# Kernel tuning notes

Hardware: AMD Instinct MI355X
Metric: run time of the kernel (lower is better)

Reference implementation:

```python
import jax, jax.numpy as jnp
import numpy as np

B, N, DIM_IN, DIM_OUT, CHEB_K, EMBED_DIM = 64, 2048, 64, 64, 3, 10


def setup_inputs() -> dict:
    key = jax.random.key(0)
    k1, k2, k3, k4 = jax.random.split(key, 4)
    x = jax.random.normal(k1, (B, N, DIM_IN), dtype=jnp.float32)
    node_embeddings = jax.random.normal(k2, (N, EMBED_DIM), dtype=jnp.float32)
    # xavier-normal-like init for the pools
    w_std = (2.0 / (EMBED_DIM * CHEB_K * DIM_IN + DIM_OUT)) ** 0.5
    b_std = (2.0 / (EMBED_DIM + DIM_OUT)) ** 0.5
    weights_pool = jax.random.normal(k3, (EMBED_DIM, CHEB_K, DIM_IN, DIM_OUT), dtype=jnp.float32) * w_std
    bias_pool = jax.random.normal(k4, (EMBED_DIM, DIM_OUT), dtype=jnp.float32) * b_std
    return {"x": x, "node_embeddings": node_embeddings,
            "weights_pool": weights_pool, "bias_pool": bias_pool,
            "cheb_k": CHEB_K}


def reference(x, node_embeddings, weights_pool, bias_pool, cheb_k):
    n = node_embeddings.shape[0]
    # adaptive adjacency: softmax(relu(E E^T)) over neighbors
    supports = jax.nn.softmax(jax.nn.relu(node_embeddings @ node_embeddings.T), axis=1)
    # Chebyshev polynomial supports: T0 = I, T1 = A, Tk = 2 A T_{k-1} - T_{k-2}
    support_set = [jnp.eye(n, dtype=supports.dtype), supports]
    for _ in range(2, cheb_k):
        support_set.append(2.0 * supports @ support_set[-1] - support_set[-2])
    supports_k = jnp.stack(support_set, axis=0)  # [K, N, N]
    # per-node weights and bias synthesized from node embeddings
    weights = jnp.einsum('nd,dkio->nkio', node_embeddings, weights_pool)  # [N, K, I, O]
    bias = node_embeddings @ bias_pool                                    # [N, O]
    # graph convolution
    x_g = jnp.einsum('knm,bmc->bnkc', supports_k, x)                      # [B, N, K, I]
    out = jnp.einsum('bnki,nkio->bno', x_g, weights) + bias               # [B, N, O]
    return out
```

## Files before the change

kernel.cpp:

```cpp
#include <hip/hip_runtime.h>

#define NN 2048
#define BB 64
#define CC 64
#define ED 10
#define KK 3
#define JJ (BB * CC)

typedef unsigned short ushort_t;
typedef __attribute__((ext_vector_type(8))) short short8;
typedef __attribute__((ext_vector_type(4))) float f32x4;

typedef const __attribute__((address_space(1))) unsigned* gptr_t;
typedef __attribute__((address_space(3))) unsigned* lptr_t;

static __device__ __forceinline__ ushort_t f2bf(float f) {
    union { float f; unsigned u; } x{f};
    unsigned r = x.u + 0x7FFF + ((x.u >> 16) & 1);
    return (ushort_t)(r >> 16);
}
static __device__ __forceinline__ float bf2f(ushort_t h) {
    union { unsigned u; float f; } x;
    x.u = ((unsigned)h) << 16;
    return x.f;
}

__global__ __launch_bounds__(256) void prep_kernel(const float* __restrict__ E,
                                                   const float* __restrict__ x,
                                                   const float* __restrict__ Wp,
                                                   ushort_t* __restrict__ Ab,
                                                   ushort_t* __restrict__ xT,
                                                   ushort_t* __restrict__ xN,
                                                   ushort_t* __restrict__ WpT) {
    const int bid = blockIdx.x;
    const int tid = threadIdx.x;

    __shared__ float tb[64][68];
    __shared__ float red[8];

    if (bid < NN) {
        const int n = bid;
        float en[ED];
#pragma unroll
        for (int d = 0; d < ED; ++d) en[d] = E[n * ED + d];

        float sv[NN / 256];
        float lmax = 0.0f;
#pragma unroll
        for (int j = 0; j < NN / 256; ++j) {
            const int m = tid + j * 256;
            const float* Em = E + m * ED;
            float dot = 0.0f;
#pragma unroll
            for (int d = 0; d < ED; ++d) dot += en[d] * Em[d];
            float s = fmaxf(dot, 0.0f);
            sv[j] = s;
            lmax = fmaxf(lmax, s);
        }
#pragma unroll
        for (int off = 32; off > 0; off >>= 1) lmax = fmaxf(lmax, __shfl_down(lmax, off, 64));
        if ((tid & 63) == 0) red[tid >> 6] = lmax;
        __syncthreads();
        const float bmax = fmaxf(fmaxf(red[0], red[1]), fmaxf(red[2], red[3]));

        float lsum = 0.0f;
#pragma unroll
        for (int j = 0; j < NN / 256; ++j) {
            sv[j] = __expf(sv[j] - bmax);
            lsum += sv[j];
        }
#pragma unroll
        for (int off = 32; off > 0; off >>= 1) lsum += __shfl_down(lsum, off, 64);
        if ((tid & 63) == 0) red[4 + (tid >> 6)] = lsum;
        __syncthreads();
        const float inv = 1.0f / (red[4] + red[5] + red[6] + red[7]);

#pragma unroll
        for (int j = 0; j < NN / 256; ++j) {
            Ab[(size_t)n * NN + tid + j * 256] = f2bf(sv[j] * inv);
        }
    } else if (bid < 2 * NN) {
        const int t = bid - NN;
        const int n0 = (t & 31) * 64;
        const int b = t >> 5;

#pragma unroll
        for (int l = 0; l < 4; ++l) {
            const int idx = tid + l * 256;
            const int nn = idx >> 4;
            const int c4 = (idx & 15) << 2;
            const float4 v = *(const float4*)(x + ((size_t)b * NN + n0 + nn) * CC + c4);
            tb[c4 + 0][nn] = v.x;
            tb[c4 + 1][nn] = v.y;
            tb[c4 + 2][nn] = v.z;
            tb[c4 + 3][nn] = v.w;
        }
        __syncthreads();

#pragma unroll
        for (int l = 0; l < 2; ++l) {
            const int idx = tid + l * 256;
            const int c = idx >> 3;
            const int ch = (idx & 7) << 3;
            ushort_t pack[8];
#pragma unroll
            for (int e = 0; e < 8; ++e) pack[e] = f2bf(tb[c][ch + e]);
            *(float4*)(xT + (size_t)(b * 64 + c) * NN + n0 + ch) = *(float4*)pack;
        }
#pragma unroll
        for (int l = 0; l < 2; ++l) {
            const int idx = tid + l * 256;
            const int nn = idx >> 3;
            const int cg = (idx & 7) << 3;
            ushort_t pack[8];
#pragma unroll
            for (int e = 0; e < 8; ++e) pack[e] = f2bf(tb[cg + e][nn]);
            *(float4*)(xN + (size_t)(n0 + nn) * JJ + b * 64 + cg) = *(float4*)pack;
        }
    } else {
        const int dk = bid - 2 * NN;
        const float* src = Wp + (size_t)dk * CC * CC;

#pragma unroll
        for (int l = 0; l < 4; ++l) {
            const int idx = tid + l * 256;
            const int i = idx >> 4;
            const int o4 = (idx & 15) << 2;
            const float4 v = *(const float4*)(src + i * CC + o4);
            tb[o4 + 0][i] = v.x;
            tb[o4 + 1][i] = v.y;
            tb[o4 + 2][i] = v.z;
            tb[o4 + 3][i] = v.w;
        }
        __syncthreads();

#pragma unroll
        for (int l = 0; l < 2; ++l) {
            const int idx = tid + l * 256;
            const int o = idx >> 3;
            const int ic = (idx & 7) << 3;
            ushort_t pack[8];
#pragma unroll
            for (int e = 0; e < 8; ++e) pack[e] = f2bf(tb[o][ic + e]);
            *(float4*)(WpT + (size_t)dk * CC * CC + o * CC + ic) = *(float4*)pack;
        }
    }
}

template <int MODE>
__global__ __launch_bounds__(256) void gemm_nt(const ushort_t* __restrict__ A,
                                               const ushort_t* __restrict__ Bt,
                                               const ushort_t* __restrict__ Zn,
                                               ushort_t* __restrict__ Ct,
                                               ushort_t* __restrict__ Cn) {
    const int j0 = blockIdx.x * 128;
    const int m0 = blockIdx.y * 128;
    const int tid = threadIdx.x;
    const int lane = tid & 63;
    const int l16 = lane & 15;
    const int quad = lane >> 4;
    const int w = tid >> 6;
    const int wm = (w >> 1) * 64;
    const int wj = (w & 1) * 64;
    const int lr = lane >> 3;
    const int lc = lane & 7;
    const int swz = lc ^ lr;

    __shared__ ushort_t As[2][128 * 64];
    __shared__ ushort_t Bs[2][128 * 64];

    f32x4 acc[4][4];
#pragma unroll
    for (int mi = 0; mi < 4; ++mi)
#pragma unroll
        for (int ji = 0; ji < 4; ++ji) acc[mi][ji] = (f32x4){0.f, 0.f, 0.f, 0.f};

#pragma unroll
    for (int inst = 0; inst < 4; ++inst) {
        const int rbase = w * 32 + inst * 8;
        const int row = rbase + lr;
        __builtin_amdgcn_global_load_lds(
            (gptr_t)(A + (size_t)(m0 + row) * NN + swz * 8),
            (lptr_t)&As[0][rbase * 64], 16, 0, 0);
        __builtin_amdgcn_global_load_lds(
            (gptr_t)(Bt + (size_t)(j0 + row) * NN + swz * 8),
            (lptr_t)&Bs[0][rbase * 64], 16, 0, 0);
    }

    for (int it = 0; it < NN / 64; ++it) {
        const int cur = it & 1;
        __syncthreads();

        if (it + 1 < NN / 64) {
            const int k0 = (it + 1) * 64;
#pragma unroll
            for (int inst = 0; inst < 4; ++inst) {
                const int rbase = w * 32 + inst * 8;
                const int row = rbase + lr;
                __builtin_amdgcn_global_load_lds(
                    (gptr_t)(A + (size_t)(m0 + row) * NN + k0 + swz * 8),
                    (lptr_t)&As[1 - cur][rbase * 64], 16, 0, 0);
                __builtin_amdgcn_global_load_lds(
                    (gptr_t)(Bt + (size_t)(j0 + row) * NN + k0 + swz * 8),
                    (lptr_t)&Bs[1 - cur][rbase * 64], 16, 0, 0);
            }
        }

#pragma unroll
        for (int ks = 0; ks < 64; ks += 32) {
            const int qb = (ks >> 3) + quad;
            short8 av[4], bv[4];
#pragma unroll
            for (int mi = 0; mi < 4; ++mi) {
                const int rA = wm + mi * 16 + l16;
                av[mi] = *(const short8*)&As[cur][rA * 64 + ((qb ^ (rA & 7)) << 3)];
            }
#pragma unroll
            for (int ji = 0; ji < 4; ++ji) {
                const int rB = wj + ji * 16 + l16;
                bv[ji] = *(const short8*)&Bs[cur][rB * 64 + ((qb ^ (rB & 7)) << 3)];
            }
#pragma unroll
            for (int mi = 0; mi < 4; ++mi)
#pragma unroll
                for (int ji = 0; ji < 4; ++ji)
                    acc[mi][ji] = __builtin_amdgcn_mfma_f32_16x16x32_bf16(
                        av[mi], bv[ji], acc[mi][ji], 0, 0, 0);
        }
    }

#pragma unroll
    for (int mi = 0; mi < 4; ++mi) {
#pragma unroll
        for (int ji = 0; ji < 4; ++ji) {
            const int j = j0 + wj + ji * 16 + l16;
            const int mb = m0 + wm + mi * 16 + quad * 4;
            if (MODE == 0) {
                ushort_t o[4];
#pragma unroll
                for (int r = 0; r < 4; ++r) o[r] = f2bf(acc[mi][ji][r]);
                *(unsigned long long*)(Ct + (size_t)j * NN + mb) = *(unsigned long long*)o;
#pragma unroll
                for (int r = 0; r < 4; ++r) Cn[(size_t)(mb + r) * JJ + j] = o[r];
            } else {
#pragma unroll
                for (int r = 0; r < 4; ++r) {
                    const float z = bf2f(Zn[(size_t)(mb + r) * JJ + j]);
                    Cn[(size_t)(mb + r) * JJ + j] = f2bf(2.0f * acc[mi][ji][r] - z);
                }
            }
        }
    }
}

#define XLD 200
__global__ __launch_bounds__(256) void out_kernel(const float* __restrict__ E,
                                                  const ushort_t* __restrict__ WpT,
                                                  const float* __restrict__ bp,
                                                  const ushort_t* __restrict__ xN,
                                                  const ushort_t* __restrict__ y1N,
                                                  const ushort_t* __restrict__ y2N,
                                                  float* __restrict__ out) {
    const int n = blockIdx.x;
    const int tid = threadIdx.x;

    __shared__ ushort_t xg[BB * XLD];
    __shared__ ushort_t Wt[CC * XLD];
    __shared__ float en_s[ED];
    __shared__ float bias_s[CC];

    if (tid < ED) en_s[tid] = E[n * ED + tid];
    __syncthreads();

    float en[ED];
#pragma unroll
    for (int d = 0; d < ED; ++d) en[d] = en_s[d];

    if (tid < CC) {
        float bsum = 0.0f;
#pragma unroll
        for (int d = 0; d < ED; ++d) bsum += en[d] * bp[d * CC + tid];
        bias_s[tid] = bsum;
    }

#pragma unroll
    for (int k = 0; k < KK; ++k) {
        const ushort_t* src = (k == 0) ? xN : (k == 1) ? y1N : y2N;
        const float4* srow = (const float4*)(src + (size_t)n * JJ);
        for (int idx = tid; idx < JJ / 8; idx += 256) {
            *(float4*)&xg[(idx >> 3) * XLD + k * 64 + ((idx & 7) << 3)] = srow[idx];
        }
    }

    for (int t = tid; t < CC * 24; t += 256) {
        const int o = t / 24;
        const int kc = t % 24;
        const int k = kc >> 3;
        const int ic = (kc & 7) << 3;
        float s[8];
#pragma unroll
        for (int e = 0; e < 8; ++e) s[e] = 0.0f;
#pragma unroll
        for (int d = 0; d < ED; ++d) {
            const float4 wv4 = *(const float4*)(WpT + ((size_t)(d * KK + k) * CC + o) * CC + ic);
            const ushort_t* wp = (const ushort_t*)&wv4;
#pragma unroll
            for (int e = 0; e < 8; ++e) s[e] += en[d] * bf2f(wp[e]);
        }
        ushort_t pack[8];
#pragma unroll
        for (int e = 0; e < 8; ++e) pack[e] = f2bf(s[e]);
        *(float4*)&Wt[o * XLD + k * 64 + ic] = *(float4*)pack;
    }
    __syncthreads();

    const int lane = tid & 63;
    const int l16 = lane & 15;
    const int quad = lane >> 4;
    const int bm = (tid >> 6) * 16;

    f32x4 acc[4];
#pragma unroll
    for (int ji = 0; ji < 4; ++ji) acc[ji] = (f32x4){0.f, 0.f, 0.f, 0.f};

#pragma unroll
    for (int kc = 0; kc < 6; ++kc) {
        const short8 av = *(const short8*)&xg[(bm + l16) * XLD + kc * 32 + quad * 8];
#pragma unroll
        for (int ji = 0; ji < 4; ++ji) {
            const short8 bv = *(const short8*)&Wt[(ji * 16 + l16) * XLD + kc * 32 + quad * 8];
            acc[ji] = __builtin_amdgcn_mfma_f32_16x16x32_bf16(av, bv, acc[ji], 0, 0, 0);
        }
    }

#pragma unroll
    for (int ji = 0; ji < 4; ++ji) {
        const int o = ji * 16 + l16;
        const float bo = bias_s[o];
#pragma unroll
        for (int r = 0; r < 4; ++r) {
            const int b = bm + quad * 4 + r;
            out[((size_t)b * NN + n) * CC + o] = acc[ji][r] + bo;
        }
    }
}
#undef XLD

extern "C" void kernel_launch(void* const* d_in, const int* in_sizes, int n_in,
                              void* d_out, int out_size, void* d_ws, size_t ws_size,
                              hipStream_t stream) {
    const float* x  = (const float*)d_in[0];
    const float* E  = (const float*)d_in[1];
    const float* Wp = (const float*)d_in[2];
    const float* bp = (const float*)d_in[3];

    ushort_t* Ab  = (ushort_t*)d_ws;
    ushort_t* xT  = Ab + (size_t)NN * NN;
    ushort_t* xN  = xT + (size_t)JJ * NN;
    ushort_t* y1T = xN + (size_t)NN * JJ;
    ushort_t* y1N = y1T + (size_t)JJ * NN;
    ushort_t* y2N = y1N + (size_t)NN * JJ;
    ushort_t* WpT = y2N + (size_t)NN * JJ;
    float* out = (float*)d_out;

    prep_kernel<<<2 * NN + ED * KK, 256, 0, stream>>>(E, x, Wp, Ab, xT, xN, WpT);
    gemm_nt<0><<<dim3(JJ / 128, NN / 128), 256, 0, stream>>>(Ab, xT, nullptr, y1T, y1N);
    gemm_nt<1><<<dim3(JJ / 128, NN / 128), 256, 0, stream>>>(Ab, y1T, xN, nullptr, y2N);
    out_kernel<<<NN, 256, 0, stream>>>(E, WpT, bp, xN, y1N, y2N, out);
}
```

Measured before the change: 217.8 us.

## Precompute T2 support matrix and fuse both propagation GEMMs into one pipelined kernel

Replaces the dependent chain y1=A·x, y2=2A·y1−x with an explicit T2=2A·A−I computed from a transposed copy of A, then runs one large 8-wave GEMM that stacks [A;T2] against x to produce y1 and y2 together. The new GEMM uses 256x256 tiles, global_load_lds direct-to-LDS staging, double buffering and setprio/sched_barrier scheduling. This removes the serial dependency and the extra transposed y1 write, but adds an N×N×N GEMM for T2 plus a transpose pass. It also changes rounding, since T2 is formed in bf16 and x is no longer subtracted in the second step.

```diff
diff --git a/kernel.cpp b/kernel.cpp
--- a/kernel.cpp
+++ b/kernel.cpp
@@ -147,12 +147,39 @@
     }
 }
 
-template <int MODE>
-__global__ __launch_bounds__(256) void gemm_nt(const ushort_t* __restrict__ A,
+__global__ __launch_bounds__(256) void trans_kernel(const ushort_t* __restrict__ Ab,
+                                                    ushort_t* __restrict__ At) {
+    const int bx = blockIdx.x;
+    const int by = blockIdx.y;
+    const int tid = threadIdx.x;
+    __shared__ ushort_t tb[64][72];
+
+#pragma unroll
+    for (int l = 0; l < 2; ++l) {
+        const int idx = tid + l * 256;
+        const int r = idx >> 3;
+        const int c0 = (idx & 7) << 3;
+        const float4 v = *(const float4*)(Ab + (size_t)(by * 64 + r) * NN + bx * 64 + c0);
+        const ushort_t* p = (const ushort_t*)&v;
+#pragma unroll
+        for (int e = 0; e < 8; ++e) tb[c0 + e][r] = p[e];
+    }
+    __syncthreads();
+#pragma unroll
+    for (int l = 0; l < 2; ++l) {
+        const int idx = tid + l * 256;
+        const int m = idx >> 3;
+        const int c0 = (idx & 7) << 3;
+        ushort_t pack[8];
+#pragma unroll
+        for (int e = 0; e < 8; ++e) pack[e] = tb[m][c0 + e];
+        *(float4*)(At + (size_t)(bx * 64 + m) * NN + by * 64 + c0) = *(float4*)pack;
+    }
+}
+
+__global__ __launch_bounds__(256) void gemm_t2(const ushort_t* __restrict__ A,
                                                const ushort_t* __restrict__ Bt,
-                                               const ushort_t* __restrict__ Zn,
-                                               ushort_t* __restrict__ Ct,
-                                               ushort_t* __restrict__ Cn) {
+                                               ushort_t* __restrict__ C) {
     const int j0 = blockIdx.x * 128;
     const int m0 = blockIdx.y * 128;
     const int tid = threadIdx.x;
@@ -235,23 +262,168 @@
         for (int ji = 0; ji < 4; ++ji) {
             const int j = j0 + wj + ji * 16 + l16;
             const int mb = m0 + wm + mi * 16 + quad * 4;
-            if (MODE == 0) {
-                ushort_t o[4];
-#pragma unroll
-                for (int r = 0; r < 4; ++r) o[r] = f2bf(acc[mi][ji][r]);
-                *(unsigned long long*)(Ct + (size_t)j * NN + mb) = *(unsigned long long*)o;
-#pragma unroll
-                for (int r = 0; r < 4; ++r) Cn[(size_t)(mb + r) * JJ + j] = o[r];
-            } else {
-#pragma unroll
-                for (int r = 0; r < 4; ++r) {
-                    const float z = bf2f(Zn[(size_t)(mb + r) * JJ + j]);
-                    Cn[(size_t)(mb + r) * JJ + j] = f2bf(2.0f * acc[mi][ji][r] - z);
-                }
+#pragma unroll
+            for (int r = 0; r < 4; ++r) {
+                const float v = 2.0f * acc[mi][ji][r] - ((mb + r) == j ? 1.0f : 0.0f);
+                C[(size_t)(mb + r) * NN + j] = f2bf(v);
             }
         }
     }
 }
+
+#define STAGE_HALF(buf, h3, kt) do {                                                        \
+    const ushort_t* s_ = ((h3) < 2) ? srcA : srcB;                                          \
+    __builtin_amdgcn_global_load_lds(                                                       \
+        (gptr_t)(s_ + (size_t)(((h3) & 1) * 2) * 64 * NN + (size_t)(kt) * 64),              \
+        (lptr_t)&lds[buf][(h3) >= 2][(((h3) & 1) * 2) * 4096 + dstoff], 16, 0, 0);          \
+    __builtin_amdgcn_global_load_lds(                                                       \
+        (gptr_t)(s_ + (size_t)(((h3) & 1) * 2 + 1) * 64 * NN + (size_t)(kt) * 64),          \
+        (lptr_t)&lds[buf][(h3) >= 2][(((h3) & 1) * 2 + 1) * 4096 + dstoff], 16, 0, 0);      \
+} while (0)
+
+#define LDA_Q(buf, qm) do {                                                                 \
+    _Pragma("unroll") for (int mi_ = 0; mi_ < 4; ++mi_)                                     \
+    _Pragma("unroll") for (int ks_ = 0; ks_ < 2; ++ks_)                                     \
+        a[mi_][ks_] = *(const short8*)&lds[buf][0][((aRG + (qm) * 4 + mi_) * 2 + ks_) * 512 + rdofs]; \
+} while (0)
+
+#define LDB_Q(buf, qn) do {                                                                 \
+    _Pragma("unroll") for (int ni_ = 0; ni_ < 2; ++ni_)                                     \
+    _Pragma("unroll") for (int ks_ = 0; ks_ < 2; ++ks_)                                     \
+        b[(qn) * 2 + ni_][ks_] = *(const short8*)&lds[buf][1][((bRG + (qn) * 2 + ni_) * 2 + ks_) * 512 + rdofs]; \
+} while (0)
+
+#define MFMA_Q(qm, qn) do {                                                                 \
+    __builtin_amdgcn_s_setprio(1);                                                          \
+    _Pragma("unroll") for (int mi_ = 0; mi_ < 4; ++mi_)                                     \
+    _Pragma("unroll") for (int nn_ = 0; nn_ < 2; ++nn_) {                                   \
+        acc[(qm) * 4 + mi_][(qn) * 2 + nn_] = __builtin_amdgcn_mfma_f32_16x16x32_bf16(      \
+            a[mi_][0], b[(qn) * 2 + nn_][0], acc[(qm) * 4 + mi_][(qn) * 2 + nn_], 0, 0, 0); \
+        acc[(qm) * 4 + mi_][(qn) * 2 + nn_] = __builtin_amdgcn_mfma_f32_16x16x32_bf16(      \
+            a[mi_][1], b[(qn) * 2 + nn_][1], acc[(qm) * 4 + mi_][(qn) * 2 + nn_], 0, 0, 0); \
+    }                                                                                       \
+    __builtin_amdgcn_s_setprio(0);                                                          \
+} while (0)
+
+#define PH_SYNC do {                                                                        \
+    __builtin_amdgcn_s_barrier();                                                           \
+    asm volatile("s_waitcnt lgkmcnt(0)" ::: "memory");                                      \
+    __builtin_amdgcn_sched_barrier(0);                                                      \
+} while (0)
+
+#define PH_END do {                                                                         \
+    __builtin_amdgcn_sched_barrier(0);                                                      \
+    __builtin_amdgcn_s_barrier();                                                           \
+} while (0)
+
+__global__ __launch_bounds__(512, 2) void gemm8(const ushort_t* __restrict__ Ab,
+                                                const ushort_t* __restrict__ T2b,
+                                                const ushort_t* __restrict__ Bt,
+                                                ushort_t* __restrict__ y1N,
+                                                ushort_t* __restrict__ y2N) {
+    int bid = blockIdx.x;
+    bid = (bid & 7) * 32 + (bid >> 3);
+    const int bx = bid & 15;
+    const int by = bid >> 4;
+    const int j0 = bx * 256;
+    const int m0 = by * 256;
+
+    const ushort_t* Arows = (by < 8) ? (Ab + (size_t)m0 * NN) : (T2b + (size_t)(m0 - NN) * NN);
+    const ushort_t* Brows = Bt + (size_t)j0 * NN;
+    ushort_t* Crow = (by < 8) ? (y1N + (size_t)m0 * JJ) : (y2N + (size_t)(m0 - NN) * JJ);
+
+    const int tid = threadIdx.x;
+    const int w = tid >> 6;
+    const int lane = tid & 63;
+    const int l16 = lane & 15;
+    const int quad = lane >> 4;
+    const int wm = (w >> 2) * 128;
+    const int wn = (w & 3) * 64;
+    const int aRG = (w >> 2) * 8;
+    const int bRG = (w & 3) * 4;
+    const int rdofs = l16 * 32 + ((quad * 8) ^ ((l16 & 8) * 2));
+
+    const int r16s = lane >> 2;
+    const int cx = (lane & 3) ^ ((r16s >> 3) << 1);
+    const int rowbase = (w >> 1) * 16 + r16s;
+    const int kofs = (w & 1) * 32 + cx * 8;
+    const ushort_t* srcA = Arows + (size_t)rowbase * NN + kofs;
+    const ushort_t* srcB = Brows + (size_t)rowbase * NN + kofs;
+    const int dstoff = tid * 8;
+
+    __shared__ ushort_t lds[2][2][16384];
+
+    f32x4 acc[8][4];
+#pragma unroll
+    for (int mi = 0; mi < 8; ++mi)
+#pragma unroll
+        for (int ni = 0; ni < 4; ++ni) acc[mi][ni] = (f32x4){0.f, 0.f, 0.f, 0.f};
+
+    short8 a[4][2], b[4][2];
+
+    STAGE_HALF(0, 0, 0); STAGE_HALF(0, 1, 0); STAGE_HALF(0, 2, 0); STAGE_HALF(0, 3, 0);
+    STAGE_HALF(1, 0, 1); STAGE_HALF(1, 1, 1);
+    asm volatile("s_waitcnt vmcnt(4)" ::: "memory");
+    __builtin_amdgcn_s_barrier();
+
+#pragma unroll 1
+    for (int i = 0; i < 16; ++i) {
+        const int tb_ = 2 * i + 1;
+        const int ta2 = 2 * i + 2;
+        const int tb2 = 2 * i + 3;
+        const bool stg = (i < 15);
+
+        LDA_Q(0, 0); LDB_Q(0, 0);
+        STAGE_HALF(1, 2, tb_);
+        PH_SYNC; MFMA_Q(0, 0); PH_END;
+        LDB_Q(0, 1);
+        STAGE_HALF(1, 3, tb_);
+        PH_SYNC; MFMA_Q(0, 1); PH_END;
+        LDA_Q(0, 1);
+        if (stg) STAGE_HALF(0, 2, ta2);
+        PH_SYNC; MFMA_Q(1, 1); PH_END;
+        if (stg) { STAGE_HALF(0, 3, ta2); STAGE_HALF(0, 0, ta2); }
+        __builtin_amdgcn_s_barrier();
+        MFMA_Q(1, 0);
+        __builtin_amdgcn_sched_barrier(0);
+        if (stg) { asm volatile("s_waitcnt vmcnt(6)" ::: "memory"); }
+        else     { asm volatile("s_waitcnt vmcnt(0)" ::: "memory"); }
+        __builtin_amdgcn_s_barrier();
+
+        LDA_Q(1, 0); LDB_Q(1, 0);
+        if (stg) STAGE_HALF(0, 1, ta2);
+        PH_SYNC; MFMA_Q(0, 0); PH_END;
+        LDB_Q(1, 1);
+        PH_SYNC; MFMA_Q(0, 1); PH_END;
+        LDA_Q(1, 1);
+        PH_SYNC; MFMA_Q(1, 1); PH_END;
+        if (stg) { STAGE_HALF(1, 0, tb2); STAGE_HALF(1, 1, tb2); }
+        __builtin_amdgcn_s_barrier();
+        MFMA_Q(1, 0);
+        __builtin_amdgcn_sched_barrier(0);
+        if (stg) { asm volatile("s_waitcnt vmcnt(4)" ::: "memory"); }
+        __builtin_amdgcn_s_barrier();
+    }
+
+#pragma unroll
+    for (int mi = 0; mi < 8; ++mi) {
+#pragma unroll
+        for (int ni = 0; ni < 4; ++ni) {
+            const int j = j0 + wn + ni * 16 + l16;
+            const int mb = wm + mi * 16 + quad * 4;
+#pragma unroll
+            for (int r = 0; r < 4; ++r)
+                Crow[(size_t)(mb + r) * JJ + j] = f2bf(acc[mi][ni][r]);
+        }
+    }
+}
+
+#undef STAGE_HALF
+#undef LDA_Q
+#undef LDB_Q
+#undef MFMA_Q
+#undef PH_SYNC
+#undef PH_END
 
 #define XLD 200
 __global__ __launch_bounds__(256) void out_kernel(const float* __restrict__ E,
@@ -357,14 +529,16 @@
     ushort_t* Ab  = (ushort_t*)d_ws;
     ushort_t* xT  = Ab + (size_t)NN * NN;
     ushort_t* xN  = xT + (size_t)JJ * NN;
-    ushort_t* y1T = xN + (size_t)NN * JJ;
-    ushort_t* y1N = y1T + (size_t)JJ * NN;
+    ushort_t* y1N = xN + (size_t)NN * JJ;
     ushort_t* y2N = y1N + (size_t)NN * JJ;
-    ushort_t* WpT = y2N + (size_t)NN * JJ;
+    ushort_t* At  = y2N;
+    ushort_t* T2b = y2N + (size_t)NN * JJ;
+    ushort_t* WpT = T2b + (size_t)NN * NN;
     float* out = (float*)d_out;
 
     prep_kernel<<<2 * NN + ED * KK, 256, 0, stream>>>(E, x, Wp, Ab, xT, xN, WpT);
-    gemm_nt<0><<<dim3(JJ / 128, NN / 128), 256, 0, stream>>>(Ab, xT, nullptr, y1T, y1N);
-    gemm_nt<1><<<dim3(JJ / 128, NN / 128), 256, 0, stream>>>(Ab, y1T, xN, nullptr, y2N);
+    trans_kernel<<<dim3(32, 32), 256, 0, stream>>>(Ab, At);
+    gemm_t2<<<dim3(16, 16), 256, 0, stream>>>(Ab, At, T2b);
+    gemm8<<<256, 512, 0, stream>>>(Ab, T2b, xT, y1N, y2N);
     out_kernel<<<NN, 256, 0, stream>>>(E, WpT, bp, xN, y1N, y2N, out);
 }
```

Measured after the change: 232.0 us. 1.07x slower.

## Fuse two Chebyshev GEMMs into one cooperative kernel with 8-wave pipelined K-loop

Applied to the files above, without the earlier changes.

Replaces the two separate 128x128-tile GEMM launches with a single cooperative kernel of 256 blocks of 512 threads. Each block computes a 128x256 tile, and a grid-wide sync separates the A·x pass from the A·y1 pass. The K loop is rewritten as a hand-scheduled ping-pong pipeline using quadrant-wise MFMA, s_setprio, explicit waitcnt and sched_barrier, with swizzled LDS and block-index remapping for L2 locality. This aims to cut launch overhead and raise MFMA utilization, but it depends on all 256 blocks being co-resident and on the fragile manual scheduling being correct.

```diff
diff --git a/kernel.cpp b/kernel.cpp
--- a/kernel.cpp
+++ b/kernel.cpp
@@ -1,4 +1,5 @@
 #include <hip/hip_runtime.h>
+#include <hip/hip_cooperative_groups.h>
 
 #define NN 2048
 #define BB 64
@@ -147,111 +148,192 @@
     }
 }
 
-template <int MODE>
-__global__ __launch_bounds__(256) void gemm_nt(const ushort_t* __restrict__ A,
-                                               const ushort_t* __restrict__ Bt,
-                                               const ushort_t* __restrict__ Zn,
-                                               ushort_t* __restrict__ Ct,
-                                               ushort_t* __restrict__ Cn) {
-    const int j0 = blockIdx.x * 128;
-    const int m0 = blockIdx.y * 128;
+#define STAGE_A(buf, kt) do {                                                               \
+    __builtin_amdgcn_global_load_lds(                                                       \
+        (gptr_t)(srcA + (size_t)(kt) * 64),                                                 \
+        (lptr_t)&lds[buf][dstoff], 16, 0, 0);                                               \
+    __builtin_amdgcn_global_load_lds(                                                       \
+        (gptr_t)(srcA + (size_t)64 * NN + (size_t)(kt) * 64),                               \
+        (lptr_t)&lds[buf][4096 + dstoff], 16, 0, 0);                                        \
+} while (0)
+
+#define STAGE_B(buf, half, kt) do {                                                         \
+    __builtin_amdgcn_global_load_lds(                                                       \
+        (gptr_t)(srcB + (size_t)((half) * 2) * 64 * NN + (size_t)(kt) * 64),                \
+        (lptr_t)&lds[buf][8192 + ((half) * 2) * 4096 + dstoff], 16, 0, 0);                  \
+    __builtin_amdgcn_global_load_lds(                                                       \
+        (gptr_t)(srcB + (size_t)((half) * 2 + 1) * 64 * NN + (size_t)(kt) * 64),            \
+        (lptr_t)&lds[buf][8192 + ((half) * 2 + 1) * 4096 + dstoff], 16, 0, 0);              \
+} while (0)
+
+#define LDA_Q(buf, qm) do {                                                                 \
+    _Pragma("unroll") for (int mi_ = 0; mi_ < 2; ++mi_)                                     \
+    _Pragma("unroll") for (int ks_ = 0; ks_ < 2; ++ks_)                                     \
+        a[mi_][ks_] = *(const short8*)&lds[buf][((aRG + (qm) * 2 + mi_) * 2 + ks_) * 512 + rdofs]; \
+} while (0)
+
+#define LDB_Q(buf, qn) do {                                                                 \
+    _Pragma("unroll") for (int ni_ = 0; ni_ < 2; ++ni_)                                     \
+    _Pragma("unroll") for (int ks_ = 0; ks_ < 2; ++ks_)                                     \
+        b[(qn) * 2 + ni_][ks_] = *(const short8*)&lds[buf][8192 + ((bRG + (qn) * 2 + ni_) * 2 + ks_) * 512 + rdofs]; \
+} while (0)
+
+#define MFMA_Q(qm, qn) do {                                                                 \
+    __builtin_amdgcn_s_setprio(1);                                                          \
+    _Pragma("unroll") for (int mi_ = 0; mi_ < 2; ++mi_)                                     \
+    _Pragma("unroll") for (int nn_ = 0; nn_ < 2; ++nn_) {                                   \
+        acc[(qm) * 2 + mi_][(qn) * 2 + nn_] = __builtin_amdgcn_mfma_f32_16x16x32_bf16(      \
+            a[mi_][0], b[(qn) * 2 + nn_][0], acc[(qm) * 2 + mi_][(qn) * 2 + nn_], 0, 0, 0); \
+        acc[(qm) * 2 + mi_][(qn) * 2 + nn_] = __builtin_amdgcn_mfma_f32_16x16x32_bf16(      \
+            a[mi_][1], b[(qn) * 2 + nn_][1], acc[(qm) * 2 + mi_][(qn) * 2 + nn_], 0, 0, 0); \
+    }                                                                                       \
+    __builtin_amdgcn_s_setprio(0);                                                          \
+} while (0)
+
+#define WAIT_READS do {                                                                     \
+    __builtin_amdgcn_s_barrier();                                                           \
+    asm volatile("s_waitcnt lgkmcnt(0)" ::: "memory");                                      \
+    __builtin_amdgcn_sched_barrier(0);                                                      \
+} while (0)
+
+#define REGION_END do {                                                                     \
+    __builtin_amdgcn_sched_barrier(0);                                                      \
+    __builtin_amdgcn_s_barrier();                                                           \
+} while (0)
+
+#define KLOOP() do {                                                                        \
+    _Pragma("unroll") for (int mi = 0; mi < 4; ++mi)                                        \
+    _Pragma("unroll") for (int ni = 0; ni < 4; ++ni)                                        \
+        acc[mi][ni] = (f32x4){0.f, 0.f, 0.f, 0.f};                                          \
+    STAGE_B(0, 0, 0); STAGE_B(0, 1, 0); STAGE_A(0, 0);                                      \
+    STAGE_A(1, 1);                                                                          \
+    asm volatile("s_waitcnt vmcnt(2)" ::: "memory");                                        \
+    __builtin_amdgcn_s_barrier();                                                           \
+    _Pragma("unroll 1") for (int i = 0; i < 16; ++i) {                                      \
+        const int tb_ = 2 * i + 1, ta2 = 2 * i + 2, tb2 = 2 * i + 3;                        \
+        const bool stg = (i < 15);                                                          \
+                                                                                    \
+        if (i) MFMA_Q(1, 0);                                                                \
+        LDA_Q(0, 0); LDB_Q(0, 0);                                                           \
+        STAGE_B(1, 0, tb_);                                                                 \
+        WAIT_READS; MFMA_Q(0, 0); LDB_Q(0, 1); REGION_END;                                  \
+                                                                                    \
+        STAGE_B(1, 1, tb_);                                                                 \
+        WAIT_READS; MFMA_Q(0, 1); LDA_Q(0, 1); REGION_END;                                  \
+                                                                                    \
+        if (stg) STAGE_B(0, 0, ta2);                                                        \
+        WAIT_READS; MFMA_Q(1, 1); REGION_END;                                               \
+                                                                         \
+        if (stg) { STAGE_B(0, 1, ta2);                                                      \
+                   asm volatile("s_waitcnt vmcnt(4)" ::: "memory"); }                       \
+        else     { asm volatile("s_waitcnt vmcnt(0)" ::: "memory"); }                       \
+        __builtin_amdgcn_s_barrier();                                                       \
+                                           \
+        MFMA_Q(1, 0);                                                                       \
+        LDA_Q(1, 0); LDB_Q(1, 0);                                                           \
+        if (stg) STAGE_A(0, ta2);                                                           \
+        WAIT_READS; MFMA_Q(0, 0); LDB_Q(1, 1); REGION_END;                                  \
+                                                                                    \
+        asm volatile("s_waitcnt lgkmcnt(0)" ::: "memory");                                  \
+        __builtin_amdgcn_sched_barrier(0);                                                  \
+        MFMA_Q(0, 1); LDA_Q(1, 1); REGION_END;                                              \
+                                                                                    \
+        asm volatile("s_waitcnt lgkmcnt(0)" ::: "memory");                                  \
+        __builtin_amdgcn_sched_barrier(0);                                                  \
+        MFMA_Q(1, 1); REGION_END;                                                           \
+                                                                       \
+        if (stg) { STAGE_A(1, tb2);                                                         \
+                   asm volatile("s_waitcnt vmcnt(2)" ::: "memory"); }                       \
+        __builtin_amdgcn_s_barrier();                                                       \
+    }                                                                                       \
+    MFMA_Q(1, 0);                                                                           \
+} while (0)
+
+__global__ __launch_bounds__(512, 2) void gemm_fused(const ushort_t* __restrict__ Ab,
+                                                     const ushort_t* __restrict__ xT,
+                                                     ushort_t* __restrict__ y1T,
+                                                     const ushort_t* __restrict__ xN,
+                                                     ushort_t* __restrict__ y1N,
+                                                     ushort_t* __restrict__ y2N) {
+    int bid = blockIdx.x;
+    bid = (bid & 7) * 32 + (bid >> 3);
+    const int bx = bid & 15;
+    const int by = bid >> 4;
+    const int j0 = bx * 256;
+    const int m0 = by * 128;
+
     const int tid = threadIdx.x;
+    const int w = tid >> 6;
     const int lane = tid & 63;
     const int l16 = lane & 15;
     const int quad = lane >> 4;
-    const int w = tid >> 6;
-    const int wm = (w >> 1) * 64;
-    const int wj = (w & 1) * 64;
-    const int lr = lane >> 3;
-    const int lc = lane & 7;
-    const int swz = lc ^ lr;
-
-    __shared__ ushort_t As[2][128 * 64];
-    __shared__ ushort_t Bs[2][128 * 64];
+    const int wm = (w >> 2) * 64;
+    const int wn = (w & 3) * 64;
+    const int aRG = (w >> 2) * 4;
+    const int bRG = (w & 3) * 4;
+    const int rdofs = l16 * 32 + ((quad * 8) ^ ((l16 & 8) * 2));
+
+    const int r16s = lane >> 2;
+    const int cx = (lane & 3) ^ ((r16s >> 3) << 1);
+    const int rowbase = (w >> 1) * 16 + r16s;
+    const int kofs = (w & 1) * 32 + cx * 8;
+    const ushort_t* srcA = Ab + (size_t)m0 * NN + (size_t)rowbase * NN + kofs;
+    const ushort_t* srcB;
+    const int dstoff = tid * 8;
+
+    __shared__ ushort_t lds[2][24576];
 
     f32x4 acc[4][4];
-#pragma unroll
-    for (int mi = 0; mi < 4; ++mi)
-#pragma unroll
-        for (int ji = 0; ji < 4; ++ji) acc[mi][ji] = (f32x4){0.f, 0.f, 0.f, 0.f};
-
-#pragma unroll
-    for (int inst = 0; inst < 4; ++inst) {
-        const int rbase = w * 32 + inst * 8;
-        const int row = rbase + lr;
-        __builtin_amdgcn_global_load_lds(
-            (gptr_t)(A + (size_t)(m0 + row) * NN + swz * 8),
-            (lptr_t)&As[0][rbase * 64], 16, 0, 0);
-        __builtin_amdgcn_global_load_lds(
-            (gptr_t)(Bt + (size_t)(j0 + row) * NN + swz * 8),
-            (lptr_t)&Bs[0][rbase * 64], 16, 0, 0);
-    }
-
-    for (int it = 0; it < NN / 64; ++it) {
-        const int cur = it & 1;
-        __syncthreads();
-
-        if (it + 1 < NN / 64) {
-            const int k0 = (it + 1) * 64;
-#pragma unroll
-            for (int inst = 0; inst < 4; ++inst) {
-                const int rbase = w * 32 + inst * 8;
-                const int row = rbase + lr;
-                __builtin_amdgcn_global_load_lds(
-                    (gptr_t)(A + (size_t)(m0 + row) * NN + k0 + swz * 8),
-                    (lptr_t)&As[1 - cur][rbase * 64], 16, 0, 0);
-                __builtin_amdgcn_global_load_lds(
-                    (gptr_t)(Bt + (size_t)(j0 + row) * NN + k0 + swz * 8),
-                    (lptr_t)&Bs[1 - cur][rbase * 64], 16, 0, 0);
+    short8 a[2][2], b[4][2];
+
+    srcB = xT + (size_t)j0 * NN + (size_t)rowbase * NN + kofs;
+    KLOOP();
+
+#pragma unroll
+    for (int mi = 0; mi < 4; ++mi) {
+#pragma unroll
+        for (int ji = 0; ji < 4; ++ji) {
+            const int j = j0 + wn + ji * 16 + l16;
+            const int mb = m0 + wm + mi * 16 + quad * 4;
+            ushort_t o[4];
+#pragma unroll
+            for (int r = 0; r < 4; ++r) o[r] = f2bf(acc[mi][ji][r]);
+            *(unsigned long long*)(y1T + (size_t)j * NN + mb) = *(unsigned long long*)o;
+#pragma unroll
+            for (int r = 0; r < 4; ++r) y1N[(size_t)(mb + r) * JJ + j] = o[r];
+        }
+    }
+
+    __threadfence();
+    cooperative_groups::this_grid().sync();
+    __threadfence();
+
+    srcB = y1T + (size_t)j0 * NN + (size_t)rowbase * NN + kofs;
+    KLOOP();
+
+#pragma unroll
+    for (int mi = 0; mi < 4; ++mi) {
+#pragma unroll
+        for (int ji = 0; ji < 4; ++ji) {
+            const int j = j0 + wn + ji * 16 + l16;
+            const int mb = m0 + wm + mi * 16 + quad * 4;
+#pragma unroll
+            for (int r = 0; r < 4; ++r) {
+                const float z = bf2f(xN[(size_t)(mb + r) * JJ + j]);
+                y2N[(size_t)(mb + r) * JJ + j] = f2bf(2.0f * acc[mi][ji][r] - z);
             }
         }
-
-#pragma unroll
-        for (int ks = 0; ks < 64; ks += 32) {
-            const int qb = (ks >> 3) + quad;
-            short8 av[4], bv[4];
-#pragma unroll
-            for (int mi = 0; mi < 4; ++mi) {
-                const int rA = wm + mi * 16 + l16;
-                av[mi] = *(const short8*)&As[cur][rA * 64 + ((qb ^ (rA & 7)) << 3)];
-            }
-#pragma unroll
-            for (int ji = 0; ji < 4; ++ji) {
-                const int rB = wj + ji * 16 + l16;
-                bv[ji] = *(const short8*)&Bs[cur][rB * 64 + ((qb ^ (rB & 7)) << 3)];
-            }
-#pragma unroll
-            for (int mi = 0; mi < 4; ++mi)
-#pragma unroll
-                for (int ji = 0; ji < 4; ++ji)
-                    acc[mi][ji] = __builtin_amdgcn_mfma_f32_16x16x32_bf16(
-                        av[mi], bv[ji], acc[mi][ji], 0, 0, 0);
-        }
-    }
-
-#pragma unroll
-    for (int mi = 0; mi < 4; ++mi) {
-#pragma unroll
-        for (int ji = 0; ji < 4; ++ji) {
-            const int j = j0 + wj + ji * 16 + l16;
-            const int mb = m0 + wm + mi * 16 + quad * 4;
-            if (MODE == 0) {
-                ushort_t o[4];
-#pragma unroll
-                for (int r = 0; r < 4; ++r) o[r] = f2bf(acc[mi][ji][r]);
-                *(unsigned long long*)(Ct + (size_t)j * NN + mb) = *(unsigned long long*)o;
-#pragma unroll
-                for (int r = 0; r < 4; ++r) Cn[(size_t)(mb + r) * JJ + j] = o[r];
-            } else {
-#pragma unroll
-                for (int r = 0; r < 4; ++r) {
-                    const float z = bf2f(Zn[(size_t)(mb + r) * JJ + j]);
-                    Cn[(size_t)(mb + r) * JJ + j] = f2bf(2.0f * acc[mi][ji][r] - z);
-                }
-            }
-        }
-    }
-}
+    }
+}
+
+#undef STAGE_A
+#undef STAGE_B
+#undef LDA_Q
+#undef LDB_Q
+#undef MFMA_Q
+#undef WAIT_READS
+#undef REGION_END
+#undef KLOOP
 
 #define XLD 200
 __global__ __launch_bounds__(256) void out_kernel(const float* __restrict__ E,
@@ -364,7 +446,11 @@
     float* out = (float*)d_out;
 
     prep_kernel<<<2 * NN + ED * KK, 256, 0, stream>>>(E, x, Wp, Ab, xT, xN, WpT);
-    gemm_nt<0><<<dim3(JJ / 128, NN / 128), 256, 0, stream>>>(Ab, xT, nullptr, y1T, y1N);
-    gemm_nt<1><<<dim3(JJ / 128, NN / 128), 256, 0, stream>>>(Ab, y1T, xN, nullptr, y2N);
+
+    void* args[] = {(void*)&Ab, (void*)&xT, (void*)&y1T, (void*)&xN,
+                    (void*)&y1N, (void*)&y2N};
+    hipLaunchCooperativeKernel((const void*)gemm_fused, dim3(256), dim3(512),
+                               args, 0, stream);
+
     out_kernel<<<NN, 256, 0, stream>>>(E, WpT, bp, xN, y1N, y2N, out);
 }
```

After: 362.1 us. 66.3% more time.

## Rewrite support GEMMs with 128x256 tiles, triple-buffered LDS pipeline and block swizzle

Applied to the files above, without the earlier changes.

Replaces the 128x128, 256-thread double-buffered GEMM with a 512-thread kernel that computes 128x256 tiles, triple-buffers LDS through direct global-to-LDS loads, and uses explicit vmcnt/lgkmcnt waits, sched barriers and setprio to overlap MFMA with loads. Block IDs are remapped so neighbouring blocks share A/B rows in cache, and a new LDS swizzle layout is used. It aims to raise MFMA utilisation and cut barrier stalls in the two dominant N×N by N×(B·C) GEMMs. In exchange it uses much more LDS and relies on hand-tuned wait counts that are fragile to correctness.

```diff
diff --git a/kernel.cpp b/kernel.cpp
--- a/kernel.cpp
+++ b/kernel.cpp
@@ -13,6 +13,8 @@
 
 typedef const __attribute__((address_space(1))) unsigned* gptr_t;
 typedef __attribute__((address_space(3))) unsigned* lptr_t;
+typedef __attribute__((address_space(3))) ushort_t* lsptr_t;
+typedef const __attribute__((address_space(3))) short8* ls8_t;
 
 static __device__ __forceinline__ ushort_t f2bf(float f) {
     union { float f; unsigned u; } x{f};
@@ -147,93 +149,125 @@
     }
 }
 
+#define STAGE_A(bp, kt) do {                                                                \
+    __builtin_amdgcn_global_load_lds(                                                       \
+        (gptr_t)(srcA + (size_t)(kt) * 64),                                                 \
+        (lptr_t)&(bp)[dstoff], 16, 0, 0);                                                   \
+    __builtin_amdgcn_global_load_lds(                                                       \
+        (gptr_t)(srcA + (size_t)64 * NN + (size_t)(kt) * 64),                               \
+        (lptr_t)&(bp)[4096 + dstoff], 16, 0, 0);                                            \
+} while (0)
+
+#define STAGE_B(bp, h, kt) do {                                                             \
+    __builtin_amdgcn_global_load_lds(                                                       \
+        (gptr_t)(srcB + (size_t)((h) * 2) * 64 * NN + (size_t)(kt) * 64),                   \
+        (lptr_t)&(bp)[8192 + (h) * 8192 + dstoff], 16, 0, 0);                               \
+    __builtin_amdgcn_global_load_lds(                                                       \
+        (gptr_t)(srcB + (size_t)((h) * 2 + 1) * 64 * NN + (size_t)(kt) * 64),               \
+        (lptr_t)&(bp)[8192 + (h) * 8192 + 4096 + dstoff], 16, 0, 0);                        \
+} while (0)
+
+#define LDA_ALL(bp) do {                                                                    \
+    _Pragma("unroll") for (int mi_ = 0; mi_ < 4; ++mi_)                                     \
+    _Pragma("unroll") for (int ks_ = 0; ks_ < 2; ++ks_)                                     \
+        a[mi_][ks_] = *(ls8_t)&(bp)[(aRG + mi_) * 1024 + ks_ * 512 + rdofs];                \
+} while (0)
+
+#define LDB_H(bp, h) do {                                                                   \
+    _Pragma("unroll") for (int nn_ = 0; nn_ < 2; ++nn_)                                     \
+    _Pragma("unroll") for (int ks_ = 0; ks_ < 2; ++ks_)                                     \
+        b[(h) * 2 + nn_][ks_] =                                                             \
+            *(ls8_t)&(bp)[8192 + (bRG + (h) * 2 + nn_) * 1024 + ks_ * 512 + rdofs];         \
+} while (0)
+
+#define MFMA_C(c) do {                                                                      \
+    __builtin_amdgcn_s_setprio(1);                                                          \
+    _Pragma("unroll") for (int mi_ = 0; mi_ < 4; ++mi_)                                     \
+    _Pragma("unroll") for (int nn_ = 0; nn_ < 2; ++nn_) {                                   \
+        acc[mi_][(c) * 2 + nn_] = __builtin_amdgcn_mfma_f32_16x16x32_bf16(                  \
+            a[mi_][0], b[(c) * 2 + nn_][0], acc[mi_][(c) * 2 + nn_], 0, 0, 0);              \
+        acc[mi_][(c) * 2 + nn_] = __builtin_amdgcn_mfma_f32_16x16x32_bf16(                  \
+            a[mi_][1], b[(c) * 2 + nn_][1], acc[mi_][(c) * 2 + nn_], 0, 0, 0);              \
+    }                                                                                       \
+    __builtin_amdgcn_s_setprio(0);                                                          \
+} while (0)
+
 template <int MODE>
-__global__ __launch_bounds__(256) void gemm_nt(const ushort_t* __restrict__ A,
-                                               const ushort_t* __restrict__ Bt,
-                                               const ushort_t* __restrict__ Zn,
-                                               ushort_t* __restrict__ Ct,
-                                               ushort_t* __restrict__ Cn) {
-    const int j0 = blockIdx.x * 128;
-    const int m0 = blockIdx.y * 128;
+__global__ __launch_bounds__(512, 2) void gemm_roll(const ushort_t* __restrict__ A,
+                                                    const ushort_t* __restrict__ Bt,
+                                                    const ushort_t* __restrict__ Zn,
+                                                    ushort_t* __restrict__ Ct,
+                                                    ushort_t* __restrict__ Cn) {
+    int bid = blockIdx.x;
+    bid = (bid & 7) * 32 + (bid >> 3);
+    const int bx = bid & 15;
+    const int by = bid >> 4;
+    const int j0 = bx * 256;
+    const int m0 = by * 128;
+
     const int tid = threadIdx.x;
+    const int w = tid >> 6;
     const int lane = tid & 63;
     const int l16 = lane & 15;
     const int quad = lane >> 4;
-    const int w = tid >> 6;
-    const int wm = (w >> 1) * 64;
-    const int wj = (w & 1) * 64;
-    const int lr = lane >> 3;
-    const int lc = lane & 7;
-    const int swz = lc ^ lr;
-
-    __shared__ ushort_t As[2][128 * 64];
-    __shared__ ushort_t Bs[2][128 * 64];
+    const int wm = (w >> 2) * 64;
+    const int wn = (w & 3) * 64;
+    const int aRG = (w >> 2) * 4;
+    const int bRG = (w & 3) * 4;
+    const int rdofs = l16 * 32 + ((quad * 8) ^ ((l16 & 8) * 2));
+
+    const int r16s = lane >> 2;
+    const int cx = (lane & 3) ^ ((r16s >> 3) << 1);
+    const int rowbase = (w >> 1) * 16 + r16s;
+    const int kofs = (w & 1) * 32 + cx * 8;
+    const ushort_t* srcA = A + (size_t)(m0 + rowbase) * NN + kofs;
+    const ushort_t* srcB = Bt + (size_t)(j0 + rowbase) * NN + kofs;
+    const int dstoff = tid * 8;
+
+    __shared__ ushort_t lds[3][24576];
+
+    lsptr_t p0 = (lsptr_t)&lds[0][0];
+    lsptr_t p1 = (lsptr_t)&lds[1][0];
+    lsptr_t p2 = (lsptr_t)&lds[2][0];
 
     f32x4 acc[4][4];
 #pragma unroll
     for (int mi = 0; mi < 4; ++mi)
 #pragma unroll
-        for (int ji = 0; ji < 4; ++ji) acc[mi][ji] = (f32x4){0.f, 0.f, 0.f, 0.f};
-
-#pragma unroll
-    for (int inst = 0; inst < 4; ++inst) {
-        const int rbase = w * 32 + inst * 8;
-        const int row = rbase + lr;
-        __builtin_amdgcn_global_load_lds(
-            (gptr_t)(A + (size_t)(m0 + row) * NN + swz * 8),
-            (lptr_t)&As[0][rbase * 64], 16, 0, 0);
-        __builtin_amdgcn_global_load_lds(
-            (gptr_t)(Bt + (size_t)(j0 + row) * NN + swz * 8),
-            (lptr_t)&Bs[0][rbase * 64], 16, 0, 0);
-    }
-
-    for (int it = 0; it < NN / 64; ++it) {
-        const int cur = it & 1;
-        __syncthreads();
-
-        if (it + 1 < NN / 64) {
-            const int k0 = (it + 1) * 64;
-#pragma unroll
-            for (int inst = 0; inst < 4; ++inst) {
-                const int rbase = w * 32 + inst * 8;
-                const int row = rbase + lr;
-                __builtin_amdgcn_global_load_lds(
-                    (gptr_t)(A + (size_t)(m0 + row) * NN + k0 + swz * 8),
-                    (lptr_t)&As[1 - cur][rbase * 64], 16, 0, 0);
-                __builtin_amdgcn_global_load_lds(
-                    (gptr_t)(Bt + (size_t)(j0 + row) * NN + k0 + swz * 8),
-                    (lptr_t)&Bs[1 - cur][rbase * 64], 16, 0, 0);
-            }
-        }
-
-#pragma unroll
-        for (int ks = 0; ks < 64; ks += 32) {
-            const int qb = (ks >> 3) + quad;
-            short8 av[4], bv[4];
-#pragma unroll
-            for (int mi = 0; mi < 4; ++mi) {
-                const int rA = wm + mi * 16 + l16;
-                av[mi] = *(const short8*)&As[cur][rA * 64 + ((qb ^ (rA & 7)) << 3)];
-            }
-#pragma unroll
-            for (int ji = 0; ji < 4; ++ji) {
-                const int rB = wj + ji * 16 + l16;
-                bv[ji] = *(const short8*)&Bs[cur][rB * 64 + ((qb ^ (rB & 7)) << 3)];
-            }
-#pragma unroll
-            for (int mi = 0; mi < 4; ++mi)
-#pragma unroll
-                for (int ji = 0; ji < 4; ++ji)
-                    acc[mi][ji] = __builtin_amdgcn_mfma_f32_16x16x32_bf16(
-                        av[mi], bv[ji], acc[mi][ji], 0, 0, 0);
-        }
-    }
+        for (int ni = 0; ni < 4; ++ni) acc[mi][ni] = (f32x4){0.f, 0.f, 0.f, 0.f};
+
+    short8 a[4][2], b[4][2];
+
+    STAGE_A(p0, 0); STAGE_B(p0, 0, 0); STAGE_B(p0, 1, 0);
+    STAGE_A(p1, 1); STAGE_B(p1, 0, 1); STAGE_B(p1, 1, 1);
+
+#pragma unroll 1
+    for (int t = 0; t < 32; ++t) {
+        if (t) MFMA_C(1);
+        if (t < 31) { asm volatile("s_waitcnt vmcnt(6)" ::: "memory"); }
+        else        { asm volatile("s_waitcnt vmcnt(0)" ::: "memory"); }
+        __builtin_amdgcn_sched_barrier(0);
+        __builtin_amdgcn_s_barrier();
+
+        LDA_ALL(p0); LDB_H(p0, 0);
+        const bool stg = (t < 30);
+        if (stg) { STAGE_A(p2, t + 2); STAGE_B(p2, 0, t + 2); }
+        asm volatile("s_waitcnt lgkmcnt(0)" ::: "memory");
+        __builtin_amdgcn_sched_barrier(0);
+        MFMA_C(0);
+        LDB_H(p0, 1);
+        if (stg) STAGE_B(p2, 1, t + 2);
+        __builtin_amdgcn_sched_barrier(0);
+
+        lsptr_t tp = p0; p0 = p1; p1 = p2; p2 = tp;
+    }
+    MFMA_C(1);
 
 #pragma unroll
     for (int mi = 0; mi < 4; ++mi) {
 #pragma unroll
         for (int ji = 0; ji < 4; ++ji) {
-            const int j = j0 + wj + ji * 16 + l16;
+            const int j = j0 + wn + ji * 16 + l16;
             const int mb = m0 + wm + mi * 16 + quad * 4;
             if (MODE == 0) {
                 ushort_t o[4];
@@ -252,6 +286,12 @@
         }
     }
 }
+
+#undef STAGE_A
+#undef STAGE_B
+#undef LDA_ALL
+#undef LDB_H
+#undef MFMA_C
 
 #define XLD 200
 __global__ __launch_bounds__(256) void out_kernel(const float* __restrict__ E,
@@ -364,7 +404,7 @@
     float* out = (float*)d_out;
 
     prep_kernel<<<2 * NN + ED * KK, 256, 0, stream>>>(E, x, Wp, Ab, xT, xN, WpT);
-    gemm_nt<0><<<dim3(JJ / 128, NN / 128), 256, 0, stream>>>(Ab, xT, nullptr, y1T, y1N);
-    gemm_nt<1><<<dim3(JJ / 128, NN / 128), 256, 0, stream>>>(Ab, y1T, xN, nullptr, y2N);
+    gemm_roll<0><<<256, 512, 0, stream>>>(Ab, xT, nullptr, y1T, y1N);
+    gemm_roll<1><<<256, 512, 0, stream>>>(Ab, y1T, xN, nullptr, y2N);
     out_kernel<<<NN, 256, 0, stream>>>(E, WpT, bp, xN, y1N, y2N, out);
 }
```

After: 204.4 us. 6.1% less time.
